# Optimization experiments

Measured on AMD Instinct MI355X. Metric: run time of the kernel, lower is better.

The kernel has to match this reference:

```python
import jax, jax.numpy as jnp
import numpy as np

NUM_HEADS = 16
D_KV = 64
NUM_BUCKETS = 32
MAX_DISTANCE = 128
LN_EPS = 1e-6


def _relative_position_bucket(seq_len):
    # bidirectional T5 bucketing
    ctx = jnp.arange(seq_len)[:, None]
    mem = jnp.arange(seq_len)[None, :]
    rel = mem - ctx  # [S, S]
    nb = NUM_BUCKETS // 2
    buckets = (rel > 0).astype(jnp.int32) * nb
    rel_abs = jnp.abs(rel)
    max_exact = nb // 2
    is_small = rel_abs < max_exact
    large = max_exact + (
        jnp.log(jnp.maximum(rel_abs, 1).astype(jnp.float32) / max_exact)
        / np.log(MAX_DISTANCE / max_exact)
        * (nb - max_exact)
    ).astype(jnp.int32)
    large = jnp.minimum(large, nb - 1)
    buckets = buckets + jnp.where(is_small, rel_abs, large)
    return buckets  # [S, S] int32


def setup_inputs() -> dict:
    key = jax.random.key(0)
    ks = jax.random.split(key, 6)
    B, S, D = 2, 2048, 1024
    scale = 1.0 / np.sqrt(D)
    return {
        "hidden_states": jax.random.normal(ks[0], (B, S, D), jnp.float32),
        "ln_weight": jnp.ones((D,), jnp.float32),
        "wq": jax.random.normal(ks[1], (D, NUM_HEADS * D_KV), jnp.float32) * scale,
        "wk": jax.random.normal(ks[2], (D, NUM_HEADS * D_KV), jnp.float32) * scale,
        "wv": jax.random.normal(ks[3], (D, NUM_HEADS * D_KV), jnp.float32) * scale,
        "wo": jax.random.normal(ks[4], (NUM_HEADS * D_KV, D), jnp.float32) * scale,
        "rel_bias": jax.random.normal(ks[5], (NUM_BUCKETS, NUM_HEADS), jnp.float32) * 0.1,
    }


def reference(hidden_states, ln_weight, wq, wk, wv, wo, rel_bias):
    B, S, D = hidden_states.shape
    # T5LayerNorm: RMS norm (no mean subtraction, no bias)
    var = jnp.mean(jnp.square(hidden_states), axis=-1, keepdims=True)
    normed = hidden_states * jax.lax.rsqrt(var + LN_EPS) * ln_weight

    def proj(w):
        return (normed @ w).reshape(B, S, NUM_HEADS, D_KV).transpose(0, 2, 1, 3)

    q = proj(wq)  # [B, H, S, dk]
    k = proj(wk)
    v = proj(wv)

    # T5 does NOT scale by sqrt(d_kv)
    scores = jnp.einsum("bhqd,bhkd->bhqk", q, k)

    buckets = _relative_position_bucket(S)           # [S, S]
    pos_bias = rel_bias[buckets]                     # [S, S, H]
    pos_bias = pos_bias.transpose(2, 0, 1)[None]     # [1, H, S, S]
    scores = scores + pos_bias

    attn = jax.nn.softmax(scores, axis=-1)
    ctx = jnp.einsum("bhqk,bhkd->bhqd", attn, v)
    ctx = ctx.transpose(0, 2, 1, 3).reshape(B, S, NUM_HEADS * D_KV)
    attn_out = ctx @ wo

    # dropout in eval mode -> identity; residual add
    return hidden_states + attn_out
```

## Files before the change

kernel.cpp:

```cpp
#include <hip/hip_runtime.h>

using s4     = __attribute__((ext_vector_type(4))) short;
using s8     = __attribute__((ext_vector_type(8))) short;
using f32x4  = __attribute__((ext_vector_type(4))) float;
using f32x4u = __attribute__((ext_vector_type(4), aligned(4))) float;

__device__ __forceinline__ float bf2f(short u) {
    union { unsigned int i; float f; } c;
    c.i = ((unsigned int)(unsigned short)u) << 16;
    return c.f;
}
__device__ __forceinline__ short f2bf(float f) {
    union { float f; unsigned int i; } c; c.f = f;
    unsigned int x = c.i;
    x += 0x7fffu + ((x >> 16) & 1u);
    return (short)(x >> 16);
}
__device__ __forceinline__ unsigned int cvt_pk_bf16(float lo, float hi) {
    unsigned int r;
    asm("v_cvt_pk_bf16_f32 %0, %1, %2" : "=v"(r) : "v"(lo), "v"(hi));
    return r;
}
__device__ __forceinline__ void gload16(const short* g, const char* lds) {
    __builtin_amdgcn_global_load_lds(
        (const __attribute__((address_space(1))) unsigned int*)(unsigned long long)(const void*)g,
        (__attribute__((address_space(3))) unsigned int*)(unsigned int)(unsigned long long)(const void*)lds,
        16, 0, 0);
}

#define MFMA(a, b, c) __builtin_amdgcn_mfma_f32_16x16x32_bf16(a, b, c, 0, 0, 0)
#define LOG2E 1.4426950408889634f
#define SM_SHIFT 80.0f

__global__ __launch_bounds__(256) void convT4_kernel(const float* __restrict__ w0,
                                                     const float* __restrict__ w1,
                                                     const float* __restrict__ w2,
                                                     const float* __restrict__ w3,
                                                     short* __restrict__ oqkv,
                                                     short* __restrict__ owo) {
    __shared__ float t[64][65];
    int z = blockIdx.z;
    const float* in = (z == 0) ? w0 : (z == 1) ? w1 : (z == 2) ? w2 : w3;
    short* out = (z < 3) ? (oqkv + (size_t)z * 1048576) : owo;
    int n0 = blockIdx.x * 64, k0 = blockIdx.y * 64;
    int tx = threadIdx.x & 15, ty = threadIdx.x >> 4;
#pragma unroll
    for (int i = 0; i < 4; ++i) {
        int r = ty + i * 16;
        f32x4 v = *(const f32x4*)(in + (size_t)(k0 + r) * 1024 + n0 + tx * 4);
        t[r][tx * 4 + 0] = v[0]; t[r][tx * 4 + 1] = v[1];
        t[r][tx * 4 + 2] = v[2]; t[r][tx * 4 + 3] = v[3];
    }
    __syncthreads();
#pragma unroll
    for (int i = 0; i < 4; ++i) {
        int r = ty + i * 16;
        s4 o;
#pragma unroll
        for (int e = 0; e < 4; ++e) o[e] = f2bf(t[tx * 4 + e][r]);
        *(s4*)(out + (size_t)(n0 + r) * 1024 + k0 + tx * 4) = o;
    }
}

__global__ __launch_bounds__(256) void rmsnorm_kernel(const float* __restrict__ x,
                                                      const float* __restrict__ w,
                                                      short* __restrict__ out) {
    int row = blockIdx.x;
    int tid = threadIdx.x;
    const float* xr = x + ((size_t)row << 10);
    f32x4 v = *(const f32x4*)(xr + tid * 4);
    float ss = v[0] * v[0] + v[1] * v[1] + v[2] * v[2] + v[3] * v[3];
#pragma unroll
    for (int off = 32; off > 0; off >>= 1) ss += __shfl_down(ss, off);
    __shared__ float red[4];
    if ((tid & 63) == 0) red[tid >> 6] = ss;
    __syncthreads();
    float total = red[0] + red[1] + red[2] + red[3];
    float r = rsqrtf(total * (1.0f / 1024.0f) + 1e-6f);
    f32x4 wv = *(const f32x4*)(w + tid * 4);
    s4 o;
    o[0] = f2bf(v[0] * r * wv[0]);
    o[1] = f2bf(v[1] * r * wv[1]);
    o[2] = f2bf(v[2] * r * wv[2]);
    o[3] = f2bf(v[3] * r * wv[3]);
    *(s4*)(out + ((size_t)row << 10) + tid * 4) = o;
}

__global__ void bias_table_kernel(const float* __restrict__ rel_bias, float* __restrict__ table) {
    int idx = blockIdx.x * 256 + threadIdx.x;
    if (idx >= 4095) return;
    int rel = 2047 - idx;
    int bucket = (rel > 0) ? 16 : 0;
    int a = (rel < 0) ? -rel : rel;
    if (a < 8) {
        bucket += a;
    } else {
        float l = logf((float)a * 0.125f) / 2.772588722239781f * 8.0f;
        int large = 8 + (int)l;
        bucket += (large > 15) ? 15 : large;
    }
#pragma unroll
    for (int h = 0; h < 16; ++h)
        table[h * 4095 + idx] = rel_bias[bucket * 16 + h] * LOG2E - SM_SHIFT;
}

template<int BN, int WROWS, int WCOLS, int MODE>
__global__ __launch_bounds__(256) void gemm2(const short* __restrict__ A,
                                             const short* __restrict__ Bt,
                                             short* __restrict__ oq,
                                             short* __restrict__ ok,
                                             short* __restrict__ ov,
                                             float* __restrict__ Cf,
                                             const float* __restrict__ resid) {
    constexpr int MI = 128 / WROWS / 16;
    constexpr int NI = BN / WCOLS / 16;
    constexpr int NA = 4;
    constexpr int NB = BN / 32;
    const int K = 1024;
    __shared__ __align__(16) char lds[(128 + BN) * 128];
    char* A_base = lds;
    char* B_base = lds + 128 * 128;

    int nbx = gridDim.x;
    int nwg = nbx * gridDim.y;
    int lid = blockIdx.y * nbx + blockIdx.x;
    int nid = (lid & 7) * (nwg >> 3) + (lid >> 3);
    int m0 = (nid / nbx) << 7, n0 = (nid % nbx) * BN;

    int tid = threadIdx.x;
    int w = tid >> 6, l = tid & 63;
    int lr = l & 15, lg = l >> 4;
    int wm = (w / WCOLS) * (128 / WROWS);
    int wn = (w % WCOLS) * (BN / WCOLS);
    int sr = l >> 3;
    int cs = (l & 7) ^ sr;

    f32x4 acc[MI][NI] = {};

    for (int kk = 0; kk < K; kk += 64) {
        __syncthreads();
#pragma unroll
        for (int i = 0; i < NA; ++i) {
            int r = (w * NA + i) * 8 + sr;
            gload16(A + (size_t)(m0 + r) * K + kk + cs * 8, A_base + (w * NA + i) * 1024);
        }
#pragma unroll
        for (int i = 0; i < NB; ++i) {
            int r = (w * NB + i) * 8 + sr;
            gload16(Bt + (size_t)(n0 + r) * K + kk + cs * 8, B_base + (w * NB + i) * 1024);
        }
        __syncthreads();

        s8 af[2][MI], bfv[2][NI];
#pragma unroll
        for (int ks = 0; ks < 2; ++ks) {
            int chunk = ((ks * 4 + lg) ^ (lr & 7)) << 4;
#pragma unroll
            for (int mi = 0; mi < MI; ++mi)
                af[ks][mi] = *(const s8*)(A_base + (wm + mi * 16 + lr) * 128 + chunk);
#pragma unroll
            for (int ni = 0; ni < NI; ++ni)
                bfv[ks][ni] = *(const s8*)(B_base + (wn + ni * 16 + lr) * 128 + chunk);
        }
#pragma unroll
        for (int ks = 0; ks < 2; ++ks)
#pragma unroll
            for (int mi = 0; mi < MI; ++mi)
#pragma unroll
                for (int ni = 0; ni < NI; ++ni)
                    acc[mi][ni] = MFMA(af[ks][mi], bfv[ks][ni], acc[mi][ni]);
    }

#pragma unroll
    for (int mi = 0; mi < MI; ++mi) {
#pragma unroll
        for (int ni = 0; ni < NI; ++ni) {
#pragma unroll
            for (int j = 0; j < 4; ++j) {
                int r = m0 + wm + mi * 16 + lg * 4 + j;
                int c = n0 + wn + ni * 16 + lr;
                float v = acc[mi][ni][j];
                if (MODE == 0) {
                    size_t idx = ((size_t)r << 10) + c;
                    Cf[idx] = v + resid[idx];
                } else {
                    int b = r >> 11, sdx = r & 2047;
                    int which = c >> 10, nn = c & 1023;
                    int h = nn >> 6, d = nn & 63;
                    if (which == 0)
                        oq[(((size_t)(b * 16 + h) << 11) + sdx) * 64 + d] = f2bf(v * LOG2E);
                    else if (which == 1)
                        ok[(((size_t)(b * 16 + h) << 11) + sdx) * 64 + d] = f2bf(v);
                    else
                        ov[((size_t)((b * 16 + h) * 64 + d) << 11) + sdx] = f2bf(v);
                }
            }
        }
    }
}

__global__ __launch_bounds__(256) void attn_kernel(const short* __restrict__ Q,
                                                   const short* __restrict__ Km,
                                                   const short* __restrict__ VT,
                                                   const float* __restrict__ tabR,
                                                   short* __restrict__ ctx) {
    const int S = 2048;
    int bid = blockIdx.x;
    int qt = bid >> 5;
    int bh = ((bid & 7) << 2) | ((bid >> 3) & 3);
    int b = bh >> 4, h = bh & 15;
    const short* Qp = Q  + (size_t)bh * S * 64;
    const short* Kp = Km + (size_t)bh * S * 64;
    const short* Vp = VT + (size_t)bh * 64 * S;
    const float* tb0 = tabR + h * 4095;

    __shared__ __align__(16) short K_lds[64 * 64];
    __shared__ __align__(16) short V_lds[64 * 64];
    __shared__ __align__(16) short P_lds[4][16 * 64];

    int tid = threadIdx.x;
    int wave = tid >> 6, lane = tid & 63;
    int lr = lane & 15, lg = lane >> 4;
    int q0 = qt * 64 + wave * 16;

    const short* qrow = Qp + (size_t)(q0 + lr) * 64 + lg * 8;
    s8 qf0 = *(const s8*)(qrow);
    s8 qf1 = *(const s8*)(qrow + 32);

    s8 ones;
#pragma unroll
    for (int e = 0; e < 8; ++e) ones[e] = (short)0x3F80;

    f32x4 o_acc[4] = {};
    f32x4 o_l = {};

    int k_row = tid >> 2;
    int kc0 = (tid & 3) * 2;
    char* k_wr0 = (char*)K_lds + k_row * 128 + ((kc0 ^ (k_row & 7)) << 4);
    char* k_wr1 = (char*)K_lds + k_row * 128 + (((kc0 + 1) ^ (k_row & 7)) << 4);
    char* v_wr0 = (char*)V_lds + k_row * 128 + ((kc0 ^ (k_row & 7)) << 4);
    char* v_wr1 = (char*)V_lds + k_row * 128 + (((kc0 + 1) ^ (k_row & 7)) << 4);

    const short* kp = Kp + (size_t)k_row * 64 + (tid & 3) * 16;
    s8 kv0 = *(const s8*)kp, kv1 = *(const s8*)(kp + 8);
    const short* vp = Vp + (size_t)k_row * S + (tid & 3) * 16;
    s8 vv0 = *(const s8*)vp, vv1 = *(const s8*)(vp + 8);

    char* pbase = (char*)P_lds + wave * 2048 + lr * 128;
    int psw = lr & 7;
    const float* tbl = tb0 + (q0 + lr - lg * 4 + 2044);

    const char* kr_base = (const char*)K_lds + lr * 128;
    int kch0 = (lg ^ (lr & 7)) << 4;
    int kch1 = ((4 + lg) ^ (lr & 7)) << 4;

    for (int kt0 = 0; kt0 < S; kt0 += 64) {
        __syncthreads();
        *(s8*)k_wr0 = kv0;
        *(s8*)k_wr1 = kv1;
        *(s8*)v_wr0 = vv0;
        *(s8*)v_wr1 = vv1;
        int nt = (kt0 + 64 < S) ? kt0 + 64 : kt0;
        kv0 = *(const s8*)(kp + (size_t)nt * 64);
        kv1 = *(const s8*)(kp + (size_t)nt * 64 + 8);
        vv0 = *(const s8*)(vp + nt);
        vv1 = *(const s8*)(vp + nt + 8);
        __syncthreads();

        f32x4 sc[4];
        __builtin_amdgcn_s_setprio(1);
#pragma unroll
        for (int kt = 0; kt < 4; ++kt) {
            s8 kf0 = *(const s8*)(kr_base + kt * 2048 + kch0);
            s8 kf1 = *(const s8*)(kr_base + kt * 2048 + kch1);
            f32x4 s = {};
            s = MFMA(kf0, qf0, s);
            s = MFMA(kf1, qf1, s);
            sc[kt] = s;
        }
        __builtin_amdgcn_s_setprio(0);

#pragma unroll
        for (int kt = 0; kt < 4; ++kt) {
            f32x4u bv = *(const f32x4u*)(tbl - kt0 - kt * 16);
#pragma unroll
            for (int j = 0; j < 4; ++j) sc[kt][j] = exp2f(sc[kt][j] + bv[3 - j]);
            uint2 pv;
            pv.x = cvt_pk_bf16(sc[kt][0], sc[kt][1]);
            pv.y = cvt_pk_bf16(sc[kt][2], sc[kt][3]);
            int sw = ((kt * 2 + (lg >> 1)) ^ psw) << 4;
            *(uint2*)(pbase + sw + (lg & 1) * 8) = pv;
        }

        s8 pf0 = *(const s8*)(pbase + ((lg ^ psw) << 4));
        s8 pf1 = *(const s8*)(pbase + (((4 + lg) ^ psw) << 4));
        __builtin_amdgcn_s_setprio(1);
#pragma unroll
        for (int dt = 0; dt < 4; ++dt) {
            int d = dt * 16 + lr;
            const char* vb = (const char*)V_lds + d * 128;
            s8 vf0 = *(const s8*)(vb + ((lg ^ (lr & 7)) << 4));
            s8 vf1 = *(const s8*)(vb + (((4 + lg) ^ (lr & 7)) << 4));
            o_acc[dt] = MFMA(vf0, pf0, o_acc[dt]);
            o_acc[dt] = MFMA(vf1, pf1, o_acc[dt]);
        }
        o_l = MFMA(ones, pf0, o_l);
        o_l = MFMA(ones, pf1, o_l);
        __builtin_amdgcn_s_setprio(0);
    }

    float rl = 1.0f / o_l[0];

    short* cbase = ctx + ((size_t)(b * 2048 + q0 + lr) << 10) + h * 64 + lg * 4;
#pragma unroll
    for (int dt = 0; dt < 4; ++dt) {
        uint2 o;
        o.x = cvt_pk_bf16(o_acc[dt][0] * rl, o_acc[dt][1] * rl);
        o.y = cvt_pk_bf16(o_acc[dt][2] * rl, o_acc[dt][3] * rl);
        *(uint2*)(cbase + dt * 16) = o;
    }
}

extern "C" void kernel_launch(void* const* d_in, const int* in_sizes, int n_in,
                              void* d_out, int out_size, void* d_ws, size_t ws_size,
                              hipStream_t stream) {
    const float* hidden = (const float*)d_in[0];
    const float* ln_w   = (const float*)d_in[1];
    const float* wq     = (const float*)d_in[2];
    const float* wk     = (const float*)d_in[3];
    const float* wv     = (const float*)d_in[4];
    const float* wo     = (const float*)d_in[5];
    const float* relb   = (const float*)d_in[6];
    float* out = (float*)d_out;

    char* ws = (char*)d_ws;
    const size_t SZ  = 8388608;
    const size_t WSZ = 2097152;
    short* normed = (short*)(ws);
    short* q      = (short*)(ws + SZ);
    short* k      = (short*)(ws + 2 * SZ);
    short* vt     = (short*)(ws + 3 * SZ);
    short* ctx    = (short*)(ws + 4 * SZ);
    short* wqkv_t = (short*)(ws + 5 * SZ);
    short* wo_t   = (short*)(ws + 5 * SZ + 3 * WSZ);
    float* table  = (float*)(ws + 5 * SZ + 4 * WSZ);

    convT4_kernel<<<dim3(16, 16, 4), 256, 0, stream>>>(wq, wk, wv, wo, wqkv_t, wo_t);
    rmsnorm_kernel<<<4096, 256, 0, stream>>>(hidden, ln_w, normed);
    bias_table_kernel<<<16, 256, 0, stream>>>(relb, table);
    gemm2<128, 2, 2, 1><<<dim3(24, 32), 256, 0, stream>>>(normed, wqkv_t, q, k, vt, nullptr, nullptr);
    attn_kernel<<<1024, 256, 0, stream>>>(q, k, vt, table, ctx);
    gemm2<64, 4, 1, 0><<<dim3(16, 32), 256, 0, stream>>>(ctx, wo_t, nullptr, nullptr, nullptr, out, hidden);
}
```

Measured before the change: 229.3 us.

## Double-buffer GEMM LDS tiles and vectorize transposed V epilogue stores

The GEMM mainloop now uses two LDS buffers, issuing global-to-LDS loads for the next K tile before computing on the current one. Partial vmcnt waits and raw barriers replace the two __syncthreads per iteration. This is meant to hide global load latency behind MFMA work. The epilogue also packs four bf16 values into one 8-byte store for the transposed V output. In exchange the kernel uses twice the LDS, which can lower occupancy.

```diff
diff --git a/kernel.cpp b/kernel.cpp
--- a/kernel.cpp
+++ b/kernel.cpp
@@ -116,10 +116,9 @@
     constexpr int NI = BN / WCOLS / 16;
     constexpr int NA = 4;
     constexpr int NB = BN / 32;
+    constexpr int BUFSZ = (128 + BN) * 128;
     const int K = 1024;
-    __shared__ __align__(16) char lds[(128 + BN) * 128];
-    char* A_base = lds;
-    char* B_base = lds + 128 * 128;
+    __shared__ __align__(16) char lds[2 * BUFSZ];
 
     int nbx = gridDim.x;
     int nwg = nbx * gridDim.y;
@@ -137,30 +136,33 @@
 
     f32x4 acc[MI][NI] = {};
 
-    for (int kk = 0; kk < K; kk += 64) {
-        __syncthreads();
+    auto stage = [&](int buf, int kk) {
+        char* Ab = lds + buf * BUFSZ;
+        char* Bb = Ab + 128 * 128;
 #pragma unroll
         for (int i = 0; i < NA; ++i) {
             int r = (w * NA + i) * 8 + sr;
-            gload16(A + (size_t)(m0 + r) * K + kk + cs * 8, A_base + (w * NA + i) * 1024);
+            gload16(A + (size_t)(m0 + r) * K + kk + cs * 8, Ab + (w * NA + i) * 1024);
         }
 #pragma unroll
         for (int i = 0; i < NB; ++i) {
             int r = (w * NB + i) * 8 + sr;
-            gload16(Bt + (size_t)(n0 + r) * K + kk + cs * 8, B_base + (w * NB + i) * 1024);
-        }
-        __syncthreads();
-
+            gload16(Bt + (size_t)(n0 + r) * K + kk + cs * 8, Bb + (w * NB + i) * 1024);
+        }
+    };
+    auto compute = [&](int buf) {
+        const char* Ab = lds + buf * BUFSZ;
+        const char* Bb = Ab + 128 * 128;
         s8 af[2][MI], bfv[2][NI];
 #pragma unroll
         for (int ks = 0; ks < 2; ++ks) {
             int chunk = ((ks * 4 + lg) ^ (lr & 7)) << 4;
 #pragma unroll
             for (int mi = 0; mi < MI; ++mi)
-                af[ks][mi] = *(const s8*)(A_base + (wm + mi * 16 + lr) * 128 + chunk);
+                af[ks][mi] = *(const s8*)(Ab + (wm + mi * 16 + lr) * 128 + chunk);
 #pragma unroll
             for (int ni = 0; ni < NI; ++ni)
-                bfv[ks][ni] = *(const s8*)(B_base + (wn + ni * 16 + lr) * 128 + chunk);
+                bfv[ks][ni] = *(const s8*)(Bb + (wn + ni * 16 + lr) * 128 + chunk);
         }
 #pragma unroll
         for (int ks = 0; ks < 2; ++ks)
@@ -169,30 +171,54 @@
 #pragma unroll
                 for (int ni = 0; ni < NI; ++ni)
                     acc[mi][ni] = MFMA(af[ks][mi], bfv[ks][ni], acc[mi][ni]);
-    }
+    };
+
+    stage(0, 0);
+#pragma unroll 1
+    for (int t = 0; t < 15; ++t) {
+        stage((t + 1) & 1, (t + 1) << 6);
+        if constexpr (NA + NB == 8) asm volatile("s_waitcnt vmcnt(8)" ::: "memory");
+        else if constexpr (NA + NB == 6) asm volatile("s_waitcnt vmcnt(6)" ::: "memory");
+        else asm volatile("s_waitcnt vmcnt(0)" ::: "memory");
+        __builtin_amdgcn_sched_barrier(0);
+        __builtin_amdgcn_s_barrier();
+        compute(t & 1);
+        __builtin_amdgcn_s_barrier();
+    }
+    asm volatile("s_waitcnt vmcnt(0)" ::: "memory");
+    __builtin_amdgcn_sched_barrier(0);
+    __builtin_amdgcn_s_barrier();
+    compute(1);
 
 #pragma unroll
     for (int mi = 0; mi < MI; ++mi) {
 #pragma unroll
         for (int ni = 0; ni < NI; ++ni) {
-#pragma unroll
-            for (int j = 0; j < 4; ++j) {
-                int r = m0 + wm + mi * 16 + lg * 4 + j;
-                int c = n0 + wn + ni * 16 + lr;
-                float v = acc[mi][ni][j];
-                if (MODE == 0) {
-                    size_t idx = ((size_t)r << 10) + c;
-                    Cf[idx] = v + resid[idx];
+            int c = n0 + wn + ni * 16 + lr;
+            int r0 = m0 + wm + mi * 16 + lg * 4;
+            if (MODE == 0) {
+#pragma unroll
+                for (int j = 0; j < 4; ++j) {
+                    size_t idx = ((size_t)(r0 + j) << 10) + c;
+                    Cf[idx] = acc[mi][ni][j] + resid[idx];
+                }
+            } else {
+                int b = r0 >> 11, sdx0 = r0 & 2047;
+                int which = c >> 10, nn = c & 1023;
+                int h = nn >> 6, d = nn & 63;
+                if (which == 2) {
+                    s4 o;
+#pragma unroll
+                    for (int j = 0; j < 4; ++j) o[j] = f2bf(acc[mi][ni][j]);
+                    *(s4*)&ov[((size_t)((b * 16 + h) * 64 + d) << 11) + sdx0] = o;
+                } else if (which == 0) {
+#pragma unroll
+                    for (int j = 0; j < 4; ++j)
+                        oq[(((size_t)(b * 16 + h) << 11) + sdx0 + j) * 64 + d] = f2bf(acc[mi][ni][j] * LOG2E);
                 } else {
-                    int b = r >> 11, sdx = r & 2047;
-                    int which = c >> 10, nn = c & 1023;
-                    int h = nn >> 6, d = nn & 63;
-                    if (which == 0)
-                        oq[(((size_t)(b * 16 + h) << 11) + sdx) * 64 + d] = f2bf(v * LOG2E);
-                    else if (which == 1)
-                        ok[(((size_t)(b * 16 + h) << 11) + sdx) * 64 + d] = f2bf(v);
-                    else
-                        ov[((size_t)((b * 16 + h) * 64 + d) << 11) + sdx] = f2bf(v);
+#pragma unroll
+                    for (int j = 0; j < 4; ++j)
+                        ok[(((size_t)(b * 16 + h) << 11) + sdx0 + j) * 64 + d] = f2bf(acc[mi][ni][j]);
                 }
             }
         }
```

New measurement: 204.8 us. 1.12x faster.
